# Kernel optimization log

Hardware: AMD Instinct MI355X
Metric: run time of the kernel (lower is better)

Reference implementation:

```python
import jax, jax.numpy as jnp
import numpy as np

R = 1  # local_window_radius (kernel = 2R+1 = 3)


def setup_inputs() -> dict:
    key = jax.random.key(0)
    ks = jax.random.split(key, 4)
    b, c, h, w, v = 4, 128, 96, 192, 2
    scale = 1.0 / np.sqrt(c).astype(np.float32)
    return {
        "feature0": jax.random.normal(ks[0], (b, c, h, w), jnp.float32),
        "flow": jax.random.normal(ks[1], (b, v, h, w), jnp.float32),
        "Wq": jax.random.normal(ks[2], (c, c), jnp.float32) * scale,
        "bq": jnp.zeros((c,), jnp.float32),
        "Wk": jax.random.normal(ks[3], (c, c), jnp.float32) * scale,
        "bk": jnp.zeros((c,), jnp.float32),
    }


def _windows(x, r):
    # x: [b, C, h, w] -> [b, h, w, C, k^2], zero-padded 3x3 neighborhoods.
    # Window element order matches F.unfold: row-major over (dy, dx).
    b, C, h, w = x.shape
    xp = jnp.pad(x, ((0, 0), (0, 0), (r, r), (r, r)))
    k = 2 * r + 1
    wins = [xp[:, :, dy:dy + h, dx:dx + w] for dy in range(k) for dx in range(k)]
    return jnp.stack(wins, axis=-1).transpose(0, 2, 3, 1, 4)


def reference(feature0, flow, Wq, bq, Wk, bk):
    b, c, h, w = feature0.shape
    f = feature0.transpose(0, 2, 3, 1)              # [b,h,w,c]
    q = f @ Wq.T + bq                                # q_proj -> [b,h,w,c]
    kproj = (f @ Wk.T + bk).transpose(0, 3, 1, 2)    # k_proj -> [b,c,h,w]
    k_win = _windows(kproj, R)                       # [b,h,w,c,k2]
    v_win = _windows(flow, R)                        # [b,h,w,v,k2]
    scores = jnp.einsum('bhwc,bhwck->bhwk', q, k_win) / jnp.sqrt(jnp.asarray(c, q.dtype))
    prob = jax.nn.softmax(scores, axis=-1)           # [b,h,w,k2]
    out = jnp.einsum('bhwk,bhwvk->bhwv', prob, v_win)
    return out.transpose(0, 3, 1, 2)                 # [b,v,h,w]
```

## Files before the change

### kernel.cpp

```cpp
#include <hip/hip_runtime.h>
#include <hip/hip_bf16.h>
#include <math.h>

#define B_   4
#define C_   128
#define H_   96
#define W_   192
#define HW_  (H_*W_)

#define TH 4
#define TW 16
#define HX 18
#define HPX 108
#define SHS 136

typedef __attribute__((ext_vector_type(8))) short bf16x8;
typedef __attribute__((ext_vector_type(4))) float f32x4;

__device__ __forceinline__ unsigned short f2bf(float f) {
    __hip_bfloat16 h = __float2bfloat16(f);
    return *(unsigned short*)&h;
}
__device__ __forceinline__ float bflo(unsigned u) { return __uint_as_float(u << 16); }
__device__ __forceinline__ float bfhi(unsigned u) { return __uint_as_float(u & 0xFFFF0000u); }

__global__ __launch_bounds__(256) void prep_kernel(
    const float* __restrict__ Wq, const float* __restrict__ Wk,
    const float* __restrict__ bq, const float* __restrict__ bk,
    short* __restrict__ Apack, float* __restrict__ u2,
    float* __restrict__ v2, float* __restrict__ c0)
{
    if (blockIdx.x < 8) {
        const int rb   = blockIdx.x;
        const int t    = threadIdx.x;
        const int lane = t & 63;
        const int row  = rb * 16 + (lane & 15);
        const int colb = (t >> 6) * 32 + (lane >> 4) * 8;
        float a[8];
#pragma unroll
        for (int j = 0; j < 8; ++j) a[j] = 0.f;
#pragma unroll 2
        for (int c = 0; c < C_; c += 4) {
            float wk[4];
            float4 wv[4][2];
#pragma unroll
            for (int u = 0; u < 4; ++u) {
                wk[u] = Wk[(c + u) * C_ + row];
                wv[u][0] = *(const float4*)(Wq + (c + u) * C_ + colb);
                wv[u][1] = *(const float4*)(Wq + (c + u) * C_ + colb + 4);
            }
#pragma unroll
            for (int u = 0; u < 4; ++u) {
                a[0] = fmaf(wk[u], wv[u][0].x, a[0]); a[1] = fmaf(wk[u], wv[u][0].y, a[1]);
                a[2] = fmaf(wk[u], wv[u][0].z, a[2]); a[3] = fmaf(wk[u], wv[u][0].w, a[3]);
                a[4] = fmaf(wk[u], wv[u][1].x, a[4]); a[5] = fmaf(wk[u], wv[u][1].y, a[5]);
                a[6] = fmaf(wk[u], wv[u][1].z, a[6]); a[7] = fmaf(wk[u], wv[u][1].w, a[7]);
            }
        }
        bf16x8 v;
#pragma unroll
        for (int j = 0; j < 8; ++j) v[j] = (short)f2bf(a[j]);
        *(bf16x8*)(Apack + ((size_t)rb * 256 + t) * 8) = v;
    } else {
        const int t = threadIdx.x;
        if (t < 128) {
            float a = 0.f;
            for (int c = 0; c < C_; ++c) a = fmaf(Wk[c * C_ + t], bq[c], a);
            u2[t] = a;
        } else {
            const int i = t - 128;
            float a = 0.f;
            for (int c = 0; c < C_; ++c) a = fmaf(Wq[c * C_ + i], bk[c], a);
            v2[i] = a;
        }
        if (t == 0) {
            float a = 0.f;
            for (int c = 0; c < C_; ++c) a = fmaf(bq[c], bk[c], a);
            c0[0] = a;
        }
    }
}

__global__ __launch_bounds__(256, 4) void fused_kernel(
    const float* __restrict__ f, const short* __restrict__ Apack,
    const float* __restrict__ u2v, const float* __restrict__ v2v,
    const float* __restrict__ c0p, const float* __restrict__ flow,
    float* __restrict__ out)
{
    __shared__ unsigned short sH[HPX * SHS];
    __shared__ float sS[TH][TW][9];

    const int t    = threadIdx.x;
    const int lane = t & 63;
    const int w    = t >> 6;
    const int g    = lane >> 4, p = lane & 15;

    const int wg  = blockIdx.x;
    const int idx = (wg & 7) * 144 + (wg >> 3);
    const int b   = idx / 288;
    const int rem = idx - b * 288;
    const int ty  = rem / 12, tx = rem - ty * 12;
    const int y0  = ty * TH, x0 = tx * TW;
    const float* fb = f + (size_t)b * C_ * HW_;

#pragma unroll
    for (int it = 0; it < 7; ++it) {
        const int gi = it * 256 + t;
        if (gi < HPX * 16) {
            const int c8 = gi / HPX;
            const int px = gi - c8 * HPX;
            const int hy = px / HX;
            const int hx = px - hy * HX;
            const int gy = y0 + hy - 1, gx = x0 + hx - 1;
            bf16x8 v = {0, 0, 0, 0, 0, 0, 0, 0};
            if ((gy >= 0) && (gy < H_) && (gx >= 0) && (gx < W_)) {
                const float* src = fb + gy * W_ + gx;
#pragma unroll
                for (int j = 0; j < 8; ++j)
                    v[j] = (short)f2bf(src[(size_t)(c8 * 8 + j) * HW_]);
            }
            *(bf16x8*)(sH + px * SHS + c8 * 8) = v;
        }
    }
    __syncthreads();

    f32x4 acc[8];
#pragma unroll
    for (int rb = 0; rb < 8; ++rb) acc[rb] = (f32x4){0.f, 0.f, 0.f, 0.f};

#pragma unroll
    for (int ks = 0; ks < 4; ++ks) {
        const int hpx = (w + 1) * HX + (p + 1);
        const bf16x8 bfr = *(const bf16x8*)(sH + hpx * SHS + (ks * 4 + g) * 8);
#pragma unroll
        for (int rb = 0; rb < 8; ++rb) {
            const bf16x8 afr = *(const bf16x8*)(Apack +
                ((size_t)((rb * 4 + ks) * 64 + lane)) * 8);
            acc[rb] = __builtin_amdgcn_mfma_f32_16x16x32_bf16(afr, bfr, acc[rb], 0, 0, 0);
        }
    }

    const int L0 = ((lane & 16) << 1) | p;
    const int L1 = L0 + 16;
    uint2 pk[8];
#pragma unroll
    for (int rb = 0; rb < 8; ++rb) {
        const f32x4 uu = *(const f32x4*)(u2v + rb * 16 + g * 4);
        const f32x4 vv = acc[rb] + uu;
        pk[rb].x = (unsigned)f2bf(vv[0]) | ((unsigned)f2bf(vv[1]) << 16);
        pk[rb].y = (unsigned)f2bf(vv[2]) | ((unsigned)f2bf(vv[3]) << 16);
    }
    bf16x8 aS[4];
#pragma unroll
    for (int ks = 0; ks < 4; ++ks) {
        int dw[4];
#pragma unroll
        for (int dd = 0; dd < 4; ++dd) {
            const int v0 = (dd & 1) ? (int)pk[2 * ks].y     : (int)pk[2 * ks].x;
            const int v1 = (dd & 1) ? (int)pk[2 * ks + 1].y : (int)pk[2 * ks + 1].x;
            const int sl = (dd & 2) ? L1 : L0;
            const int w0 = __shfl(v0, sl, 64);
            const int w1 = __shfl(v1, sl, 64);
            dw[dd] = (g & 2) ? w1 : w0;
        }
        int4 qv = make_int4(dw[0], dw[1], dw[2], dw[3]);
        aS[ks] = *(bf16x8*)&qv;
    }

#pragma unroll
    for (int dy = 0; dy < 3; ++dy) {
        const int hyy = w + dy;
        f32x4 s0 = (f32x4){0.f, 0.f, 0.f, 0.f};
        f32x4 s1 = (f32x4){0.f, 0.f, 0.f, 0.f};
#pragma unroll
        for (int ks = 0; ks < 4; ++ks) {
            const int hpx0 = hyy * HX + p;
            const bf16x8 b0 = *(const bf16x8*)(sH + hpx0 * SHS + (ks * 4 + g) * 8);
            const bf16x8 b1 = *(const bf16x8*)(sH + (hpx0 + 2) * SHS + (ks * 4 + g) * 8);
            s0 = __builtin_amdgcn_mfma_f32_16x16x32_bf16(aS[ks], b0, s0, 0, 0, 0);
            s1 = __builtin_amdgcn_mfma_f32_16x16x32_bf16(aS[ks], b1, s1, 0, 0, 0);
        }
#pragma unroll
        for (int i = 0; i < 4; ++i) {
            const int x = g * 4 + i;
            const float val = (g < 2) ? s0[i] : s1[i];
            const int   d   = (g < 2) ? (p - x) : (x - p);
            const int   n9  = (g < 2) ? (dy * 3 + d) : (dy * 3 + 2 - d);
            if ((unsigned)d <= 2u) sS[w][x][n9] = val;
        }
    }

    const int r  = (lane >> 4) & 1;
    const int v  = lane >> 5;
    const int xl = lane & 15;
    const int gy = y0 + w, gx = x0 + xl;

    float beta = 0.f;
    const bool edge = (gx == 0) | (gx == W_ - 1) | (gy == 0) | (gy == H_ - 1);
    if (edge) {
        const int hpx = (w + 1) * HX + (xl + 1);
#pragma unroll
        for (int c8 = 0; c8 < 16; ++c8) {
            const uint4 hv = *(const uint4*)(sH + hpx * SHS + c8 * 8);
            const float4 va = *(const float4*)(v2v + c8 * 8);
            const float4 vb = *(const float4*)(v2v + c8 * 8 + 4);
            beta += bflo(hv.x) * va.x + bfhi(hv.x) * va.y
                  + bflo(hv.y) * va.z + bfhi(hv.y) * va.w
                  + bflo(hv.z) * vb.x + bfhi(hv.z) * vb.y
                  + bflo(hv.w) * vb.z + bfhi(hv.w) * vb.w;
        }
        beta += *c0p;
    }

    const float scale = 0.08838834764831845f;
    float sv[9], mk[9];
    int spn[9];
    float m = -1e30f;
#pragma unroll
    for (int n = 0; n < 9; ++n) {
        const int yn = gy + n / 3 - 1, xn = gx + n % 3 - 1;
        const bool ok = (yn >= 0) && (yn < H_) && (xn >= 0) && (xn < W_);
        mk[n]  = ok ? 1.f : 0.f;
        spn[n] = ok ? yn * W_ + xn : gy * W_ + gx;
        sv[n]  = ok ? (sS[w][xl][n] + beta) * scale : 0.f;
        m = fmaxf(m, sv[n]);
    }
    float e[9], sum = 0.f;
#pragma unroll
    for (int n = 0; n < 9; ++n) { e[n] = __expf(sv[n] - m); sum += e[n]; }
    const float inv = 1.f / sum;

    if (r == 0) {
        const float* f0 = flow + ((size_t)b * 2 + v) * HW_;
        float o = 0.f;
#pragma unroll
        for (int n = 0; n < 9; ++n) o += e[n] * mk[n] * f0[spn[n]];
        out[((size_t)b * 2 + v) * HW_ + gy * W_ + gx] = o * inv;
    }
}

extern "C" void kernel_launch(void* const* d_in, const int* in_sizes, int n_in,
                              void* d_out, int out_size, void* d_ws, size_t ws_size,
                              hipStream_t stream) {
    const float* f   = (const float*)d_in[0];
    const float* flw = (const float*)d_in[1];
    const float* Wq  = (const float*)d_in[2];
    const float* bq  = (const float*)d_in[3];
    const float* Wk  = (const float*)d_in[4];
    const float* bk  = (const float*)d_in[5];
    float* out = (float*)d_out;

    short* Apack = (short*)d_ws;
    float* u2    = (float*)(Apack + 128 * 128);
    float* v2    = u2 + 128;
    float* c0    = v2 + 128;

    prep_kernel<<<9, 256, 0, stream>>>(Wq, Wk, bq, bk, Apack, u2, v2, c0);
    fused_kernel<<<1152, 256, 0, stream>>>(f, Apack, u2, v2, c0, flw, out);
}
```

Baseline: 36.99 us.

## Replace shared-memory halo staging with direct register loads and overlapping tiles

The fused kernel no longer stages a bf16 halo tile of features in LDS. Each wave now loads its own row, plus the rows above and below, straight from global memory into MFMA B-fragments. Tiles become 16 columns wide with one column of overlap on each side (14 output columns each), which needs 1344 blocks and clamps at the borders. The beta bias term is now computed for every pixel with a wave reduction instead of only on edges. The prep loop is also unrolled differently. This removes the LDS fill, the barrier and the LDS traffic, at the cost of redundant global loads of neighbouring rows and overlapping columns.

```diff
diff --git a/kernel.cpp b/kernel.cpp
--- a/kernel.cpp
+++ b/kernel.cpp
@@ -8,21 +8,24 @@
 #define W_   192
 #define HW_  (H_*W_)
 
-#define TH 4
-#define TW 16
-#define HX 18
-#define HPX 108
-#define SHS 136
-
 typedef __attribute__((ext_vector_type(8))) short bf16x8;
 typedef __attribute__((ext_vector_type(4))) float f32x4;
 
-__device__ __forceinline__ unsigned short f2bf(float f) {
+__device__ __forceinline__ unsigned f2bfu(float f) {
     __hip_bfloat16 h = __float2bfloat16(f);
-    return *(unsigned short*)&h;
+    return (unsigned)*(unsigned short*)&h;
 }
 __device__ __forceinline__ float bflo(unsigned u) { return __uint_as_float(u << 16); }
 __device__ __forceinline__ float bfhi(unsigned u) { return __uint_as_float(u & 0xFFFF0000u); }
+
+__device__ __forceinline__ bf16x8 pack8(const float* v) {
+    int4 q;
+    q.x = (int)(f2bfu(v[0]) | (f2bfu(v[1]) << 16));
+    q.y = (int)(f2bfu(v[2]) | (f2bfu(v[3]) << 16));
+    q.z = (int)(f2bfu(v[4]) | (f2bfu(v[5]) << 16));
+    q.w = (int)(f2bfu(v[6]) | (f2bfu(v[7]) << 16));
+    return *(bf16x8*)&q;
+}
 
 __global__ __launch_bounds__(256) void prep_kernel(
     const float* __restrict__ Wq, const float* __restrict__ Wk,
@@ -39,27 +42,25 @@
         float a[8];
 #pragma unroll
         for (int j = 0; j < 8; ++j) a[j] = 0.f;
-#pragma unroll 2
-        for (int c = 0; c < C_; c += 4) {
-            float wk[4];
-            float4 wv[4][2];
-#pragma unroll
-            for (int u = 0; u < 4; ++u) {
+#pragma unroll 1
+        for (int c = 0; c < C_; c += 8) {
+            float  wk[8];
+            float4 w0[8], w1[8];
+#pragma unroll
+            for (int u = 0; u < 8; ++u) {
                 wk[u] = Wk[(c + u) * C_ + row];
-                wv[u][0] = *(const float4*)(Wq + (c + u) * C_ + colb);
-                wv[u][1] = *(const float4*)(Wq + (c + u) * C_ + colb + 4);
+                w0[u] = *(const float4*)(Wq + (c + u) * C_ + colb);
+                w1[u] = *(const float4*)(Wq + (c + u) * C_ + colb + 4);
             }
 #pragma unroll
-            for (int u = 0; u < 4; ++u) {
-                a[0] = fmaf(wk[u], wv[u][0].x, a[0]); a[1] = fmaf(wk[u], wv[u][0].y, a[1]);
-                a[2] = fmaf(wk[u], wv[u][0].z, a[2]); a[3] = fmaf(wk[u], wv[u][0].w, a[3]);
-                a[4] = fmaf(wk[u], wv[u][1].x, a[4]); a[5] = fmaf(wk[u], wv[u][1].y, a[5]);
-                a[6] = fmaf(wk[u], wv[u][1].z, a[6]); a[7] = fmaf(wk[u], wv[u][1].w, a[7]);
+            for (int u = 0; u < 8; ++u) {
+                a[0] = fmaf(wk[u], w0[u].x, a[0]); a[1] = fmaf(wk[u], w0[u].y, a[1]);
+                a[2] = fmaf(wk[u], w0[u].z, a[2]); a[3] = fmaf(wk[u], w0[u].w, a[3]);
+                a[4] = fmaf(wk[u], w1[u].x, a[4]); a[5] = fmaf(wk[u], w1[u].y, a[5]);
+                a[6] = fmaf(wk[u], w1[u].z, a[6]); a[7] = fmaf(wk[u], w1[u].w, a[7]);
             }
         }
-        bf16x8 v;
-#pragma unroll
-        for (int j = 0; j < 8; ++j) v[j] = (short)f2bf(a[j]);
+        bf16x8 v = pack8(a);
         *(bf16x8*)(Apack + ((size_t)rb * 256 + t) * 8) = v;
     } else {
         const int t = threadIdx.x;
@@ -87,8 +88,7 @@
     const float* __restrict__ c0p, const float* __restrict__ flow,
     float* __restrict__ out)
 {
-    __shared__ unsigned short sH[HPX * SHS];
-    __shared__ float sS[TH][TW][9];
+    __shared__ float sS[4][16][9];
 
     const int t    = threadIdx.x;
     const int lane = t & 63;
@@ -96,47 +96,37 @@
     const int g    = lane >> 4, p = lane & 15;
 
     const int wg  = blockIdx.x;
-    const int idx = (wg & 7) * 144 + (wg >> 3);
-    const int b   = idx / 288;
-    const int rem = idx - b * 288;
-    const int ty  = rem / 12, tx = rem - ty * 12;
-    const int y0  = ty * TH, x0 = tx * TW;
+    const int idx = (wg & 7) * 168 + (wg >> 3);
+    const int b   = idx / 336;
+    const int rem = idx - b * 336;
+    const int ty  = rem / 14, tx = rem - ty * 14;
+    const int y   = ty * 4 + w;
+    int x0 = tx * 14; if (x0 > W_ - 14) x0 = W_ - 14;
     const float* fb = f + (size_t)b * C_ * HW_;
 
-#pragma unroll
-    for (int it = 0; it < 7; ++it) {
-        const int gi = it * 256 + t;
-        if (gi < HPX * 16) {
-            const int c8 = gi / HPX;
-            const int px = gi - c8 * HPX;
-            const int hy = px / HX;
-            const int hx = px - hy * HX;
-            const int gy = y0 + hy - 1, gx = x0 + hx - 1;
-            bf16x8 v = {0, 0, 0, 0, 0, 0, 0, 0};
-            if ((gy >= 0) && (gy < H_) && (gx >= 0) && (gx < W_)) {
-                const float* src = fb + gy * W_ + gx;
-#pragma unroll
-                for (int j = 0; j < 8; ++j)
-                    v[j] = (short)f2bf(src[(size_t)(c8 * 8 + j) * HW_]);
-            }
-            *(bf16x8*)(sH + px * SHS + c8 * 8) = v;
-        }
-    }
-    __syncthreads();
+    const int xw = x0 - 1 + p;
+    const int xc = xw < 0 ? 0 : (xw > W_ - 1 ? W_ - 1 : xw);
+
+    bf16x8 fC[4];
+#pragma unroll
+    for (int ks = 0; ks < 4; ++ks) {
+        const float* src = fb + (size_t)(ks * 32 + g * 8) * HW_ + y * W_ + xc;
+        float v[8];
+#pragma unroll
+        for (int j = 0; j < 8; ++j) v[j] = src[(size_t)j * HW_];
+        fC[ks] = pack8(v);
+    }
 
     f32x4 acc[8];
 #pragma unroll
     for (int rb = 0; rb < 8; ++rb) acc[rb] = (f32x4){0.f, 0.f, 0.f, 0.f};
-
-#pragma unroll
-    for (int ks = 0; ks < 4; ++ks) {
-        const int hpx = (w + 1) * HX + (p + 1);
-        const bf16x8 bfr = *(const bf16x8*)(sH + hpx * SHS + (ks * 4 + g) * 8);
+#pragma unroll
+    for (int ks = 0; ks < 4; ++ks) {
 #pragma unroll
         for (int rb = 0; rb < 8; ++rb) {
             const bf16x8 afr = *(const bf16x8*)(Apack +
                 ((size_t)((rb * 4 + ks) * 64 + lane)) * 8);
-            acc[rb] = __builtin_amdgcn_mfma_f32_16x16x32_bf16(afr, bfr, acc[rb], 0, 0, 0);
+            acc[rb] = __builtin_amdgcn_mfma_f32_16x16x32_bf16(afr, fC[ks], acc[rb], 0, 0, 0);
         }
     }
 
@@ -147,8 +137,8 @@
     for (int rb = 0; rb < 8; ++rb) {
         const f32x4 uu = *(const f32x4*)(u2v + rb * 16 + g * 4);
         const f32x4 vv = acc[rb] + uu;
-        pk[rb].x = (unsigned)f2bf(vv[0]) | ((unsigned)f2bf(vv[1]) << 16);
-        pk[rb].y = (unsigned)f2bf(vv[2]) | ((unsigned)f2bf(vv[3]) << 16);
+        pk[rb].x = f2bfu(vv[0]) | (f2bfu(vv[1]) << 16);
+        pk[rb].y = f2bfu(vv[2]) | (f2bfu(vv[3]) << 16);
     }
     bf16x8 aS[4];
 #pragma unroll
@@ -169,48 +159,52 @@
 
 #pragma unroll
     for (int dy = 0; dy < 3; ++dy) {
-        const int hyy = w + dy;
-        f32x4 s0 = (f32x4){0.f, 0.f, 0.f, 0.f};
-        f32x4 s1 = (f32x4){0.f, 0.f, 0.f, 0.f};
-#pragma unroll
-        for (int ks = 0; ks < 4; ++ks) {
-            const int hpx0 = hyy * HX + p;
-            const bf16x8 b0 = *(const bf16x8*)(sH + hpx0 * SHS + (ks * 4 + g) * 8);
-            const bf16x8 b1 = *(const bf16x8*)(sH + (hpx0 + 2) * SHS + (ks * 4 + g) * 8);
-            s0 = __builtin_amdgcn_mfma_f32_16x16x32_bf16(aS[ks], b0, s0, 0, 0, 0);
-            s1 = __builtin_amdgcn_mfma_f32_16x16x32_bf16(aS[ks], b1, s1, 0, 0, 0);
-        }
+        bf16x8 fN[4];
+        if (dy == 1) {
+#pragma unroll
+            for (int ks = 0; ks < 4; ++ks) fN[ks] = fC[ks];
+        } else {
+            int yy = y + dy - 1;
+            yy = yy < 0 ? 0 : (yy > H_ - 1 ? H_ - 1 : yy);
+#pragma unroll
+            for (int ks = 0; ks < 4; ++ks) {
+                const float* src = fb + (size_t)(ks * 32 + g * 8) * HW_ + yy * W_ + xc;
+                float v[8];
+#pragma unroll
+                for (int j = 0; j < 8; ++j) v[j] = src[(size_t)j * HW_];
+                fN[ks] = pack8(v);
+            }
+        }
+        f32x4 sd = (f32x4){0.f, 0.f, 0.f, 0.f};
+#pragma unroll
+        for (int ks = 0; ks < 4; ++ks)
+            sd = __builtin_amdgcn_mfma_f32_16x16x32_bf16(aS[ks], fN[ks], sd, 0, 0, 0);
 #pragma unroll
         for (int i = 0; i < 4; ++i) {
-            const int x = g * 4 + i;
-            const float val = (g < 2) ? s0[i] : s1[i];
-            const int   d   = (g < 2) ? (p - x) : (x - p);
-            const int   n9  = (g < 2) ? (dy * 3 + d) : (dy * 3 + 2 - d);
-            if ((unsigned)d <= 2u) sS[w][x][n9] = val;
-        }
-    }
-
-    const int r  = (lane >> 4) & 1;
-    const int v  = lane >> 5;
-    const int xl = lane & 15;
-    const int gy = y0 + w, gx = x0 + xl;
-
-    float beta = 0.f;
-    const bool edge = (gx == 0) | (gx == W_ - 1) | (gy == 0) | (gy == H_ - 1);
-    if (edge) {
-        const int hpx = (w + 1) * HX + (xl + 1);
-#pragma unroll
-        for (int c8 = 0; c8 < 16; ++c8) {
-            const uint4 hv = *(const uint4*)(sH + hpx * SHS + c8 * 8);
-            const float4 va = *(const float4*)(v2v + c8 * 8);
-            const float4 vb = *(const float4*)(v2v + c8 * 8 + 4);
-            beta += bflo(hv.x) * va.x + bfhi(hv.x) * va.y
-                  + bflo(hv.y) * va.z + bfhi(hv.y) * va.w
-                  + bflo(hv.z) * vb.x + bfhi(hv.z) * vb.y
-                  + bflo(hv.w) * vb.z + bfhi(hv.w) * vb.w;
-        }
-        beta += *c0p;
-    }
+            const int row = g * 4 + i;
+            const int d1  = p - row + 1;
+            if ((unsigned)d1 <= 2u) sS[w][row][dy * 3 + d1] = sd[i];
+        }
+    }
+
+    float bl = 0.f;
+#pragma unroll
+    for (int ks = 0; ks < 4; ++ks) {
+        const f32x4 va = *(const f32x4*)(v2v + ks * 32 + g * 8);
+        const f32x4 vb = *(const f32x4*)(v2v + ks * 32 + g * 8 + 4);
+        const int4 qd = *(const int4*)&fC[ks];
+        bl += bflo((unsigned)qd.x) * va[0] + bfhi((unsigned)qd.x) * va[1]
+            + bflo((unsigned)qd.y) * va[2] + bfhi((unsigned)qd.y) * va[3]
+            + bflo((unsigned)qd.z) * vb[0] + bfhi((unsigned)qd.z) * vb[1]
+            + bflo((unsigned)qd.w) * vb[2] + bfhi((unsigned)qd.w) * vb[3];
+    }
+    bl += __shfl_xor(bl, 16, 64);
+    bl += __shfl_xor(bl, 32, 64);
+    const float beta = bl + *c0p;
+
+    const int rr = p;
+    const int vch = g >> 1;
+    const int gy = y, gx = x0 - 1 + rr;
 
     const float scale = 0.08838834764831845f;
     float sv[9], mk[9];
@@ -221,8 +215,8 @@
         const int yn = gy + n / 3 - 1, xn = gx + n % 3 - 1;
         const bool ok = (yn >= 0) && (yn < H_) && (xn >= 0) && (xn < W_);
         mk[n]  = ok ? 1.f : 0.f;
-        spn[n] = ok ? yn * W_ + xn : gy * W_ + gx;
-        sv[n]  = ok ? (sS[w][xl][n] + beta) * scale : 0.f;
+        spn[n] = ok ? yn * W_ + xn : 0;
+        sv[n]  = ok ? (sS[w][rr][n] + beta) * scale : 0.f;
         m = fmaxf(m, sv[n]);
     }
     float e[9], sum = 0.f;
@@ -230,12 +224,12 @@
     for (int n = 0; n < 9; ++n) { e[n] = __expf(sv[n] - m); sum += e[n]; }
     const float inv = 1.f / sum;
 
-    if (r == 0) {
-        const float* f0 = flow + ((size_t)b * 2 + v) * HW_;
+    if (((g & 1) == 0) && (rr >= 1) && (rr <= 14)) {
+        const float* f0 = flow + ((size_t)b * 2 + vch) * HW_;
         float o = 0.f;
 #pragma unroll
         for (int n = 0; n < 9; ++n) o += e[n] * mk[n] * f0[spn[n]];
-        out[((size_t)b * 2 + v) * HW_ + gy * W_ + gx] = o * inv;
+        out[((size_t)b * 2 + vch) * HW_ + gy * W_ + gx] = o * inv;
     }
 }
 
@@ -256,5 +250,5 @@
     float* c0    = v2 + 128;
 
     prep_kernel<<<9, 256, 0, stream>>>(Wq, Wk, bq, bk, Apack, u2, v2, c0);
-    fused_kernel<<<1152, 256, 0, stream>>>(f, Apack, u2, v2, c0, flw, out);
-}
+    fused_kernel<<<1344, 256, 0, stream>>>(f, Apack, u2, v2, c0, flw, out);
+}
```

Measured after the change: 48.84 us. 1.32x slower.

## Batch halo loads into registers, prefetch flow, permute Wq·Wk rows to drop shuffles

Applied to the files above, without the earlier changes.

The halo staging now issues all 56 global loads per thread up front into registers, with clamped addresses, before converting and writing to LDS. This aims to expose more memory-level parallelism. The flow neighbours are prefetched before the barrier. The rows of the precomputed Wk^T·Wq product are permuted in the prep kernel so the MFMA output layout already matches the A-operand layout of the second MFMA, which removes the cross-lane shuffles. Occupancy hint drops from 4 to 2 waves per SIMD to make room for the larger register footprint, which risks less latency hiding.

```diff
diff --git a/kernel.cpp b/kernel.cpp
--- a/kernel.cpp
+++ b/kernel.cpp
@@ -17,12 +17,21 @@
 typedef __attribute__((ext_vector_type(8))) short bf16x8;
 typedef __attribute__((ext_vector_type(4))) float f32x4;
 
-__device__ __forceinline__ unsigned short f2bf(float f) {
+__device__ __forceinline__ unsigned f2bfu(float f) {
     __hip_bfloat16 h = __float2bfloat16(f);
-    return *(unsigned short*)&h;
+    return (unsigned)*(unsigned short*)&h;
 }
 __device__ __forceinline__ float bflo(unsigned u) { return __uint_as_float(u << 16); }
 __device__ __forceinline__ float bfhi(unsigned u) { return __uint_as_float(u & 0xFFFF0000u); }
+
+__device__ __forceinline__ bf16x8 pack8(const float* v) {
+    int4 q;
+    q.x = (int)(f2bfu(v[0]) | (f2bfu(v[1]) << 16));
+    q.y = (int)(f2bfu(v[2]) | (f2bfu(v[3]) << 16));
+    q.z = (int)(f2bfu(v[4]) | (f2bfu(v[5]) << 16));
+    q.w = (int)(f2bfu(v[6]) | (f2bfu(v[7]) << 16));
+    return *(bf16x8*)&q;
+}
 
 __global__ __launch_bounds__(256) void prep_kernel(
     const float* __restrict__ Wq, const float* __restrict__ Wk,
@@ -34,32 +43,31 @@
         const int rb   = blockIdx.x;
         const int t    = threadIdx.x;
         const int lane = t & 63;
-        const int row  = rb * 16 + (lane & 15);
+        const int r    = lane & 15;
+        const int row  = (rb >> 1) * 32 + (r >> 2) * 8 + (rb & 1) * 4 + (r & 3);
         const int colb = (t >> 6) * 32 + (lane >> 4) * 8;
         float a[8];
 #pragma unroll
         for (int j = 0; j < 8; ++j) a[j] = 0.f;
-#pragma unroll 2
-        for (int c = 0; c < C_; c += 4) {
-            float wk[4];
-            float4 wv[4][2];
-#pragma unroll
-            for (int u = 0; u < 4; ++u) {
+#pragma unroll 1
+        for (int c = 0; c < C_; c += 8) {
+            float  wk[8];
+            float4 w0[8], w1[8];
+#pragma unroll
+            for (int u = 0; u < 8; ++u) {
                 wk[u] = Wk[(c + u) * C_ + row];
-                wv[u][0] = *(const float4*)(Wq + (c + u) * C_ + colb);
-                wv[u][1] = *(const float4*)(Wq + (c + u) * C_ + colb + 4);
+                w0[u] = *(const float4*)(Wq + (c + u) * C_ + colb);
+                w1[u] = *(const float4*)(Wq + (c + u) * C_ + colb + 4);
             }
 #pragma unroll
-            for (int u = 0; u < 4; ++u) {
-                a[0] = fmaf(wk[u], wv[u][0].x, a[0]); a[1] = fmaf(wk[u], wv[u][0].y, a[1]);
-                a[2] = fmaf(wk[u], wv[u][0].z, a[2]); a[3] = fmaf(wk[u], wv[u][0].w, a[3]);
-                a[4] = fmaf(wk[u], wv[u][1].x, a[4]); a[5] = fmaf(wk[u], wv[u][1].y, a[5]);
-                a[6] = fmaf(wk[u], wv[u][1].z, a[6]); a[7] = fmaf(wk[u], wv[u][1].w, a[7]);
+            for (int u = 0; u < 8; ++u) {
+                a[0] = fmaf(wk[u], w0[u].x, a[0]); a[1] = fmaf(wk[u], w0[u].y, a[1]);
+                a[2] = fmaf(wk[u], w0[u].z, a[2]); a[3] = fmaf(wk[u], w0[u].w, a[3]);
+                a[4] = fmaf(wk[u], w1[u].x, a[4]); a[5] = fmaf(wk[u], w1[u].y, a[5]);
+                a[6] = fmaf(wk[u], w1[u].z, a[6]); a[7] = fmaf(wk[u], w1[u].w, a[7]);
             }
         }
-        bf16x8 v;
-#pragma unroll
-        for (int j = 0; j < 8; ++j) v[j] = (short)f2bf(a[j]);
+        bf16x8 v = pack8(a);
         *(bf16x8*)(Apack + ((size_t)rb * 256 + t) * 8) = v;
     } else {
         const int t = threadIdx.x;
@@ -81,7 +89,7 @@
     }
 }
 
-__global__ __launch_bounds__(256, 4) void fused_kernel(
+__global__ __launch_bounds__(256, 2) void fused_kernel(
     const float* __restrict__ f, const short* __restrict__ Apack,
     const float* __restrict__ u2v, const float* __restrict__ v2v,
     const float* __restrict__ c0p, const float* __restrict__ flow,
@@ -103,31 +111,53 @@
     const int y0  = ty * TH, x0 = tx * TW;
     const float* fb = f + (size_t)b * C_ * HW_;
 
+    float stg[7][8];
+    bool  okv[7];
+#pragma unroll
+    for (int it = 0; it < 7; ++it) {
+        int gi = it * 256 + t; if (gi > HPX * 16 - 1) gi = HPX * 16 - 1;
+        const int c8 = gi / HPX;
+        const int px = gi - c8 * HPX;
+        const int hy = px / HX;
+        const int hx = px - hy * HX;
+        const int gy = y0 + hy - 1, gx = x0 + hx - 1;
+        const bool ok = (gy >= 0) && (gy < H_) && (gx >= 0) && (gx < W_);
+        okv[it] = ok;
+        const int gyc = ok ? gy : 0, gxc = ok ? gx : 0;
+        const float* src = fb + (size_t)(c8 * 8) * HW_ + gyc * W_ + gxc;
+#pragma unroll
+        for (int j = 0; j < 8; ++j) stg[it][j] = src[(size_t)j * HW_];
+    }
 #pragma unroll
     for (int it = 0; it < 7; ++it) {
         const int gi = it * 256 + t;
         if (gi < HPX * 16) {
             const int c8 = gi / HPX;
             const int px = gi - c8 * HPX;
-            const int hy = px / HX;
-            const int hx = px - hy * HX;
-            const int gy = y0 + hy - 1, gx = x0 + hx - 1;
-            bf16x8 v = {0, 0, 0, 0, 0, 0, 0, 0};
-            if ((gy >= 0) && (gy < H_) && (gx >= 0) && (gx < W_)) {
-                const float* src = fb + gy * W_ + gx;
-#pragma unroll
-                for (int j = 0; j < 8; ++j)
-                    v[j] = (short)f2bf(src[(size_t)(c8 * 8 + j) * HW_]);
-            }
-            *(bf16x8*)(sH + px * SHS + c8 * 8) = v;
-        }
+            float v[8];
+#pragma unroll
+            for (int j = 0; j < 8; ++j) v[j] = okv[it] ? stg[it][j] : 0.f;
+            *(bf16x8*)(sH + px * SHS + c8 * 8) = pack8(v);
+        }
+    }
+
+    const int xl = lane & 15;
+    const int gy = y0 + w, gx = x0 + xl;
+    const int vch = g >> 1;
+    float mk[9], flw9[9];
+#pragma unroll
+    for (int n = 0; n < 9; ++n) {
+        const int yn = gy + n / 3 - 1, xn = gx + n % 3 - 1;
+        const bool ok = (yn >= 0) && (yn < H_) && (xn >= 0) && (xn < W_);
+        mk[n] = ok ? 1.f : 0.f;
+        const int spn = ok ? yn * W_ + xn : gy * W_ + gx;
+        flw9[n] = flow[((size_t)b * 2 + vch) * HW_ + spn];
     }
     __syncthreads();
 
     f32x4 acc[8];
 #pragma unroll
     for (int rb = 0; rb < 8; ++rb) acc[rb] = (f32x4){0.f, 0.f, 0.f, 0.f};
-
 #pragma unroll
     for (int ks = 0; ks < 4; ++ks) {
         const int hpx = (w + 1) * HX + (p + 1);
@@ -140,30 +170,19 @@
         }
     }
 
-    const int L0 = ((lane & 16) << 1) | p;
-    const int L1 = L0 + 16;
     uint2 pk[8];
 #pragma unroll
     for (int rb = 0; rb < 8; ++rb) {
-        const f32x4 uu = *(const f32x4*)(u2v + rb * 16 + g * 4);
+        const f32x4 uu = *(const f32x4*)(u2v + (rb >> 1) * 32 + g * 8 + (rb & 1) * 4);
         const f32x4 vv = acc[rb] + uu;
-        pk[rb].x = (unsigned)f2bf(vv[0]) | ((unsigned)f2bf(vv[1]) << 16);
-        pk[rb].y = (unsigned)f2bf(vv[2]) | ((unsigned)f2bf(vv[3]) << 16);
+        pk[rb].x = f2bfu(vv[0]) | (f2bfu(vv[1]) << 16);
+        pk[rb].y = f2bfu(vv[2]) | (f2bfu(vv[3]) << 16);
     }
     bf16x8 aS[4];
 #pragma unroll
     for (int ks = 0; ks < 4; ++ks) {
-        int dw[4];
-#pragma unroll
-        for (int dd = 0; dd < 4; ++dd) {
-            const int v0 = (dd & 1) ? (int)pk[2 * ks].y     : (int)pk[2 * ks].x;
-            const int v1 = (dd & 1) ? (int)pk[2 * ks + 1].y : (int)pk[2 * ks + 1].x;
-            const int sl = (dd & 2) ? L1 : L0;
-            const int w0 = __shfl(v0, sl, 64);
-            const int w1 = __shfl(v1, sl, 64);
-            dw[dd] = (g & 2) ? w1 : w0;
-        }
-        int4 qv = make_int4(dw[0], dw[1], dw[2], dw[3]);
+        const int4 qv = make_int4((int)pk[2 * ks].x, (int)pk[2 * ks].y,
+                                  (int)pk[2 * ks + 1].x, (int)pk[2 * ks + 1].y);
         aS[ks] = *(bf16x8*)&qv;
     }
 
@@ -189,11 +208,6 @@
             if ((unsigned)d <= 2u) sS[w][x][n9] = val;
         }
     }
-
-    const int r  = (lane >> 4) & 1;
-    const int v  = lane >> 5;
-    const int xl = lane & 15;
-    const int gy = y0 + w, gx = x0 + xl;
 
     float beta = 0.f;
     const bool edge = (gx == 0) | (gx == W_ - 1) | (gy == 0) | (gy == H_ - 1);
@@ -213,29 +227,23 @@
     }
 
     const float scale = 0.08838834764831845f;
-    float sv[9], mk[9];
-    int spn[9];
+    float sv[9], e[9];
     float m = -1e30f;
 #pragma unroll
     for (int n = 0; n < 9; ++n) {
-        const int yn = gy + n / 3 - 1, xn = gx + n % 3 - 1;
-        const bool ok = (yn >= 0) && (yn < H_) && (xn >= 0) && (xn < W_);
-        mk[n]  = ok ? 1.f : 0.f;
-        spn[n] = ok ? yn * W_ + xn : gy * W_ + gx;
-        sv[n]  = ok ? (sS[w][xl][n] + beta) * scale : 0.f;
+        sv[n] = (mk[n] != 0.f) ? (sS[w][xl][n] + beta) * scale : 0.f;
         m = fmaxf(m, sv[n]);
     }
-    float e[9], sum = 0.f;
+    float sum = 0.f;
 #pragma unroll
     for (int n = 0; n < 9; ++n) { e[n] = __expf(sv[n] - m); sum += e[n]; }
     const float inv = 1.f / sum;
 
-    if (r == 0) {
-        const float* f0 = flow + ((size_t)b * 2 + v) * HW_;
+    if ((g & 1) == 0) {
         float o = 0.f;
 #pragma unroll
-        for (int n = 0; n < 9; ++n) o += e[n] * mk[n] * f0[spn[n]];
-        out[((size_t)b * 2 + v) * HW_ + gy * W_ + gx] = o * inv;
+        for (int n = 0; n < 9; ++n) o += e[n] * mk[n] * flw9[n];
+        out[((size_t)b * 2 + vch) * HW_ + gy * W_ + gx] = o * inv;
     }
 }
 
```

Result: slower. 40.61 us (+9.8%).
